# Optimization experiments

Measured on AMD Instinct MI355X. Metric: run time of the kernel, lower is better.

## Reference

```python
import jax, jax.numpy as jnp
import numpy as np

B, L, D = 4096, 16, 256  # batch, feat_len, feat_dim
N_ENC = 2                # common + synergy encoders


def _layer_norm(x, gamma, beta, eps=1e-5):
    m = jnp.mean(x, axis=-1, keepdims=True)
    v = jnp.mean(jnp.square(x - m), axis=-1, keepdims=True)
    return (x - m) * jax.lax.rsqrt(v + eps) * gamma + beta


def _estimator(gin, pin, Wg, bg, gng, gnb, Wp, bp, png, pnb, wga, bga, wpa, bpa):
    # MLP_Block = Linear + LayerNorm (Dropout is identity at inference)
    g = _layer_norm(jnp.einsum('bld,ed->ble', gin, Wg) + bg, gng, gnb)  # [B,L,D]
    p = _layer_norm(jnp.einsum('bld,ed->ble', pin, Wp) + bp, png, pnb)  # [B,L,D]
    # atten[b,l,i,j] = g[b,l,i]*p[b,l,j]
    # Linear(D,1) over j: sum_j wga_j*g_i*p_j + bga = g_i*(p.wga) + bga  (fused, no [B,L,D,D])
    geno_att = jax.nn.sigmoid(g * jnp.einsum('bld,d->bl', p, wga)[..., None] + bga)
    # permuted copy: atten.T over last two dims, Linear over i: p_j*(g.wpa) + bpa
    path_att = jax.nn.sigmoid(p * jnp.einsum('bld,d->bl', g, wpa)[..., None] + bpa)
    return p * path_att + g * geno_att


def setup_inputs() -> dict:
    key = jax.random.key(0)
    ks = jax.random.split(key, 8)
    s = 1.0 / np.sqrt(D)
    inp = {
        'gfeat': jax.random.normal(ks[0], (B, L, D), jnp.float32),
        'pfeat': jax.random.normal(ks[1], (B, L, D), jnp.float32),
        # stacked params for the 2 encoders (common, synergy)
        'Wg': jax.random.normal(ks[2], (N_ENC, D, D), jnp.float32) * s,
        'bg': jnp.zeros((N_ENC, D), jnp.float32),
        'gng': jnp.ones((N_ENC, D), jnp.float32),
        'gnb': jnp.zeros((N_ENC, D), jnp.float32),
        'Wp': jax.random.normal(ks[3], (N_ENC, D, D), jnp.float32) * s,
        'bp': jnp.zeros((N_ENC, D), jnp.float32),
        'png': jnp.ones((N_ENC, D), jnp.float32),
        'pnb': jnp.zeros((N_ENC, D), jnp.float32),
        'wga': jax.random.normal(ks[4], (N_ENC, D), jnp.float32) * s,
        'bga': jnp.zeros((N_ENC,), jnp.float32),
        'wpa': jax.random.normal(ks[5], (N_ENC, D), jnp.float32) * s,
        'bpa': jnp.zeros((N_ENC,), jnp.float32),
    }
    return inp


def reference(gfeat, pfeat, Wg, bg, gng, gnb, Wp, bp, png, pnb, wga, bga, wpa, bpa):
    # Knowledge_Decomposition calls both encoders as encoder(pfeat, gfeat) (swapped)
    est = jax.vmap(_estimator, in_axes=(None, None) + (0,) * 12)
    out = est(pfeat, gfeat, Wg, bg, gng, gnb, Wp, bp, png, pnb, wga, bga, wpa, bpa)  # [2,B,L,D]
    return (out[0], out[1])  # (common, synergy)
```

## Files before the change

### kernel.cpp

```cpp
#include <hip/hip_runtime.h>
#include <stdint.h>

typedef __bf16 bf16x8 __attribute__((ext_vector_type(8)));
typedef float  f32x4  __attribute__((ext_vector_type(4)));

#define BLD   16777216
#define DDIM  256

#define PARAM_OFF 0
#define STATS_OFF 8192
#define ROWC_OFF  16384
#define CONST_OFF 18432
#define SMEM_BYTES 18448

__device__ __forceinline__ float sigmoid_fast(float x){
  float e = __builtin_amdgcn_exp2f(-1.44269504f * x);
  return __builtin_amdgcn_rcpf(1.0f + e);
}

__device__ __forceinline__ bf16x8 cvt8(const float* p){
  float4 a = *(const float4*)p;
  float4 b = *(const float4*)(p + 4);
  bf16x8 r;
  r[0]=(__bf16)a.x; r[1]=(__bf16)a.y; r[2]=(__bf16)a.z; r[3]=(__bf16)a.w;
  r[4]=(__bf16)b.x; r[5]=(__bf16)b.y; r[6]=(__bf16)b.z; r[7]=(__bf16)b.w;
  return r;
}

__device__ __forceinline__ float ldp(const unsigned char* sm, int arr, int col){
  return ((const float*)(sm + PARAM_OFF))[arr*256 + col];
}

__global__ __launch_bounds__(256, 2)
void kd_kernel(const float* __restrict__ gfeat, const float* __restrict__ pfeat,
               const float* __restrict__ Wg,  const float* __restrict__ bg,
               const float* __restrict__ gng, const float* __restrict__ gnb,
               const float* __restrict__ Wp,  const float* __restrict__ bp,
               const float* __restrict__ pngm,const float* __restrict__ pnb,
               const float* __restrict__ wga, const float* __restrict__ bga,
               const float* __restrict__ wpa, const float* __restrict__ bpa,
               float* __restrict__ out)
{
  __shared__ __align__(16) unsigned char sm[SMEM_BYTES];
  const int tid  = threadIdx.x;
  const int n    = tid & 15;
  const int q    = (tid >> 4) & 3;
  const int w    = tid >> 6;
  const int tile = blockIdx.x >> 1;
  const int e    = blockIdx.x & 1;

  {
    float* pp = (float*)(sm + PARAM_OFF);
    pp[0*256 + tid] = bg  [e*256 + tid];
    pp[1*256 + tid] = gng [e*256 + tid];
    pp[2*256 + tid] = gnb [e*256 + tid];
    pp[3*256 + tid] = bp  [e*256 + tid];
    pp[4*256 + tid] = pngm[e*256 + tid];
    pp[5*256 + tid] = pnb [e*256 + tid];
    pp[6*256 + tid] = wga [e*256 + tid];
    pp[7*256 + tid] = wpa [e*256 + tid];
  }
  __syncthreads();

  if (tid < 64){
    float c0=0.f, c1=0.f, c2=0.f, c3=0.f;
    #pragma unroll
    for (int j = 0; j < 4; ++j){
      int c = tid*4 + j;
      float gng_ = ldp(sm,1,c), gnb_ = ldp(sm,2,c);
      float png_ = ldp(sm,4,c), pnb_ = ldp(sm,5,c);
      float wga_ = ldp(sm,6,c), wpa_ = ldp(sm,7,c);
      c0 += gng_*wpa_; c1 += gnb_*wpa_; c2 += png_*wga_; c3 += pnb_*wga_;
    }
    #pragma unroll
    for (int m = 1; m <= 32; m <<= 1){
      c0 += __shfl_xor(c0,m); c1 += __shfl_xor(c1,m);
      c2 += __shfl_xor(c2,m); c3 += __shfl_xor(c3,m);
    }
    if (tid == 0){
      float* cp = (float*)(sm + CONST_OFF);
      cp[0]=c0; cp[1]=c1; cp[2]=c2; cp[3]=c3;
    }
  }

  const float* aGbase = pfeat + (size_t)(tile*64 + n)*DDIM + q*8;
  const float* aPbase = gfeat + (size_t)(tile*64 + n)*DDIM + q*8;

  f32x4 accg[4][4], accp[4][4];
  #pragma unroll
  for (int t = 0; t < 4; ++t){
    int col = w*64 + n*4 + t;
    float bgv = ldp(sm,0,col);
    float bpv = ldp(sm,3,col);
    #pragma unroll
    for (int s = 0; s < 4; ++s){
      accg[s][t] = (f32x4){bgv,bgv,bgv,bgv};
      accp[s][t] = (f32x4){bpv,bpv,bpv,bpv};
    }
  }

  const float* wgE = Wg + (size_t)e*65536;
  const float* wpE = Wp + (size_t)e*65536;
  const float* wgR[4];
  const float* wpR[4];
  #pragma unroll
  for (int t = 0; t < 4; ++t){
    int row = w*64 + n*4 + t;
    wgR[t] = wgE + (size_t)row*DDIM + q*8;
    wpR[t] = wpE + (size_t)row*DDIM + q*8;
  }

  for (int kk = 0; kk < 8; ++kk){
    bf16x8 aG[4], aP[4], bG[4], bP[4];
    #pragma unroll
    for (int s = 0; s < 4; ++s){
      aG[s] = cvt8(aGbase + (size_t)s*16*DDIM + kk*32);
      aP[s] = cvt8(aPbase + (size_t)s*16*DDIM + kk*32);
    }
    #pragma unroll
    for (int t = 0; t < 4; ++t){
      bG[t] = cvt8(wgR[t] + kk*32);
      bP[t] = cvt8(wpR[t] + kk*32);
    }
    #pragma unroll
    for (int s = 0; s < 4; ++s){
      #pragma unroll
      for (int t = 0; t < 4; ++t){
        accg[s][t] = __builtin_amdgcn_mfma_f32_16x16x32_bf16(aG[s], bG[t], accg[s][t], 0,0,0);
        accp[s][t] = __builtin_amdgcn_mfma_f32_16x16x32_bf16(aP[s], bP[t], accp[s][t], 0,0,0);
      }
    }
  }

  float gamg[4], betg[4], gamp[4], betp[4], gwk[4], pwk[4];
  #pragma unroll
  for (int t = 0; t < 4; ++t){
    int col = w*64 + n*4 + t;
    float gng_ = ldp(sm,1,col), gnb_ = ldp(sm,2,col);
    float png_ = ldp(sm,4,col), pnb_ = ldp(sm,5,col);
    float wga_ = ldp(sm,6,col), wpa_ = ldp(sm,7,col);
    gamg[t]=gng_; betg[t]=gnb_; gamp[t]=png_; betp[t]=pnb_;
    gwk[t]=gng_*wpa_;
    pwk[t]=png_*wga_;
  }

  #pragma unroll
  for (int s = 0; s < 4; ++s){
    #pragma unroll
    for (int reg = 0; reg < 4; ++reg){
      float gs=0.f,gq=0.f,gw=0.f,ps=0.f,pq=0.f,pw=0.f;
      #pragma unroll
      for (int t = 0; t < 4; ++t){
        float xg = accg[s][t][reg], xp = accp[s][t][reg];
        gs += xg; gq = fmaf(xg,xg,gq); gw = fmaf(xg,gwk[t],gw);
        ps += xp; pq = fmaf(xp,xp,pq); pw = fmaf(xp,pwk[t],pw);
      }
      #pragma unroll
      for (int m = 1; m <= 8; m <<= 1){
        gs += __shfl_xor(gs,m); gq += __shfl_xor(gq,m); gw += __shfl_xor(gw,m);
        ps += __shfl_xor(ps,m); pq += __shfl_xor(pq,m); pw += __shfl_xor(pw,m);
      }
      if (n == 0){
        int r = s*16 + q*4 + reg;
        float* st = (float*)(sm + STATS_OFF) + (r*4 + w)*8;
        st[0]=gs; st[1]=gq; st[2]=gw; st[3]=ps; st[4]=pq; st[5]=pw;
      }
    }
  }
  __syncthreads();

  if (tid < 64){
    const float* cs = (const float*)(sm + CONST_OFF);
    float gs=0.f,gq=0.f,gw=0.f,ps=0.f,pq=0.f,pw=0.f;
    #pragma unroll
    for (int w2 = 0; w2 < 4; ++w2){
      const float* st = (const float*)(sm + STATS_OFF) + (tid*4 + w2)*8;
      gs+=st[0]; gq+=st[1]; gw+=st[2]; ps+=st[3]; pq+=st[4]; pw+=st[5];
    }
    float mg = gs*(1.f/256.f), vg = fmaxf(gq*(1.f/256.f) - mg*mg, 0.f);
    float rsg = rsqrtf(vg + 1e-5f);
    float mp = ps*(1.f/256.f), vp = fmaxf(pq*(1.f/256.f) - mp*mp, 0.f);
    float rsp = rsqrtf(vp + 1e-5f);
    float sp = rsg*(gw - mg*cs[0]) + cs[1];
    float sg = rsp*(pw - mp*cs[2]) + cs[3];
    float* rc = (float*)(sm + ROWC_OFF) + tid*8;
    rc[0]=mg; rc[1]=rsg; rc[2]=mp; rc[3]=rsp; rc[4]=sg; rc[5]=sp;
  }
  __syncthreads();

  const float bgaf = bga[e];
  const float bpaf = bpa[e];
  #pragma unroll
  for (int s = 0; s < 4; ++s){
    #pragma unroll
    for (int reg = 0; reg < 4; ++reg){
      int r = s*16 + q*4 + reg;
      const float* rc = (const float*)(sm + ROWC_OFF) + r*8;
      float mg=rc[0], rsg=rc[1], mp=rc[2], rsp=rc[3], sg=rc[4], sp=rc[5];
      float4 o;
      float ov[4];
      #pragma unroll
      for (int t = 0; t < 4; ++t){
        float g_ln = fmaf((accg[s][t][reg]-mg)*rsg, gamg[t], betg[t]);
        float p_ln = fmaf((accp[s][t][reg]-mp)*rsp, gamp[t], betp[t]);
        float ga = sigmoid_fast(fmaf(g_ln, sg, bgaf));
        float pa = sigmoid_fast(fmaf(p_ln, sp, bpaf));
        ov[t] = p_ln*pa + g_ln*ga;
      }
      o.x = ov[0]; o.y = ov[1]; o.z = ov[2]; o.w = ov[3];
      size_t off = (size_t)e*BLD + ((size_t)tile*64 + r)*DDIM + (w*64 + n*4);
      *(float4*)(out + off) = o;
    }
  }
}

extern "C" void kernel_launch(void* const* d_in, const int* in_sizes, int n_in,
                              void* d_out, int out_size, void* d_ws, size_t ws_size,
                              hipStream_t stream) {
  const float* gfeat = (const float*)d_in[0];
  const float* pfeat = (const float*)d_in[1];
  const float* Wg    = (const float*)d_in[2];
  const float* bg    = (const float*)d_in[3];
  const float* gng   = (const float*)d_in[4];
  const float* gnb   = (const float*)d_in[5];
  const float* Wp    = (const float*)d_in[6];
  const float* bp    = (const float*)d_in[7];
  const float* pngm  = (const float*)d_in[8];
  const float* pnb   = (const float*)d_in[9];
  const float* wga   = (const float*)d_in[10];
  const float* bga   = (const float*)d_in[11];
  const float* wpa   = (const float*)d_in[12];
  const float* bpa   = (const float*)d_in[13];

  dim3 grid(2048), block(256);
  hipLaunchKernelGGL(kd_kernel, grid, block, 0, stream,
                     gfeat, pfeat, Wg, bg, gng, gnb, Wp, bp, pngm, pnb,
                     wga, bga, wpa, bpa, (float*)d_out);
}
```

Before: 537.8 us.

## Stage activation tile in swizzled LDS as bf16 and halve rows per block

Each block now handles 32 rows instead of 64, doubling the grid. The block's activation tile is loaded once, converted to bf16 and stored in LDS with an XOR swizzle, and the MFMA A-fragments are read from LDS instead of being re-fetched from global memory per wave. The occupancy hint rises to 3 blocks per CU. The cost is a larger LDS footprint and an extra barrier. Weights are now re-read from global/L2 twice as often overall because tiles are smaller.

```diff
diff --git a/kernel.cpp b/kernel.cpp
--- a/kernel.cpp
+++ b/kernel.cpp
@@ -7,11 +7,13 @@
 #define BLD   16777216
 #define DDIM  256
 
-#define PARAM_OFF 0
-#define STATS_OFF 8192
-#define ROWC_OFF  16384
-#define CONST_OFF 18432
-#define SMEM_BYTES 18448
+#define AG_OFF    0
+#define AP_OFF    16384
+#define PARAM_OFF 32768
+#define STATS_OFF 40960
+#define ROWC_OFF  45056
+#define CONST_OFF 46080
+#define SMEM_BYTES 46096
 
 __device__ __forceinline__ float sigmoid_fast(float x){
   float e = __builtin_amdgcn_exp2f(-1.44269504f * x);
@@ -31,7 +33,7 @@
   return ((const float*)(sm + PARAM_OFF))[arr*256 + col];
 }
 
-__global__ __launch_bounds__(256, 2)
+__global__ __launch_bounds__(256, 3)
 void kd_kernel(const float* __restrict__ gfeat, const float* __restrict__ pfeat,
                const float* __restrict__ Wg,  const float* __restrict__ bg,
                const float* __restrict__ gng, const float* __restrict__ gnb,
@@ -49,6 +51,9 @@
   const int tile = blockIdx.x >> 1;
   const int e    = blockIdx.x & 1;
 
+  const int q16  = q*16;
+  const int xorv = (n & 7) << 4;
+
   {
     float* pp = (float*)(sm + PARAM_OFF);
     pp[0*256 + tid] = bg  [e*256 + tid];
@@ -60,6 +65,22 @@
     pp[6*256 + tid] = wga [e*256 + tid];
     pp[7*256 + tid] = wpa [e*256 + tid];
   }
+
+  {
+    const float* srcG = pfeat + (size_t)tile*32*DDIM;
+    const float* srcP = gfeat + (size_t)tile*32*DDIM;
+    #pragma unroll
+    for (int j = 0; j < 4; ++j){
+      int idx = j*2048 + tid*8;
+      int row = idx >> 8;
+      int col = idx & 255;
+      bf16x8 vg = cvt8(srcG + idx);
+      bf16x8 vp = cvt8(srcP + idx);
+      int off = row*512 + ((col*2) ^ ((row & 7) << 4));
+      *(bf16x8*)(sm + AG_OFF + off) = vg;
+      *(bf16x8*)(sm + AP_OFF + off) = vp;
+    }
+  }
   __syncthreads();
 
   if (tid < 64){
@@ -83,17 +104,14 @@
     }
   }
 
-  const float* aGbase = pfeat + (size_t)(tile*64 + n)*DDIM + q*8;
-  const float* aPbase = gfeat + (size_t)(tile*64 + n)*DDIM + q*8;
-
-  f32x4 accg[4][4], accp[4][4];
+  f32x4 accg[2][4], accp[2][4];
   #pragma unroll
   for (int t = 0; t < 4; ++t){
     int col = w*64 + n*4 + t;
     float bgv = ldp(sm,0,col);
     float bpv = ldp(sm,3,col);
     #pragma unroll
-    for (int s = 0; s < 4; ++s){
+    for (int s = 0; s < 2; ++s){
       accg[s][t] = (f32x4){bgv,bgv,bgv,bgv};
       accp[s][t] = (f32x4){bpv,bpv,bpv,bpv};
     }
@@ -101,29 +119,26 @@
 
   const float* wgE = Wg + (size_t)e*65536;
   const float* wpE = Wp + (size_t)e*65536;
-  const float* wgR[4];
-  const float* wpR[4];
-  #pragma unroll
-  for (int t = 0; t < 4; ++t){
-    int row = w*64 + n*4 + t;
-    wgR[t] = wgE + (size_t)row*DDIM + q*8;
-    wpR[t] = wpE + (size_t)row*DDIM + q*8;
-  }
+  int woff[4];
+  #pragma unroll
+  for (int t = 0; t < 4; ++t)
+    woff[t] = (w*64 + n*4 + t)*DDIM + q*8;
 
   for (int kk = 0; kk < 8; ++kk){
-    bf16x8 aG[4], aP[4], bG[4], bP[4];
-    #pragma unroll
-    for (int s = 0; s < 4; ++s){
-      aG[s] = cvt8(aGbase + (size_t)s*16*DDIM + kk*32);
-      aP[s] = cvt8(aPbase + (size_t)s*16*DDIM + kk*32);
+    bf16x8 aG[2], aP[2], bG[4], bP[4];
+    #pragma unroll
+    for (int s = 0; s < 2; ++s){
+      int off = (s*16 + n)*512 + ((kk*64 + q16) ^ xorv);
+      aG[s] = *(const bf16x8*)(sm + AG_OFF + off);
+      aP[s] = *(const bf16x8*)(sm + AP_OFF + off);
     }
     #pragma unroll
     for (int t = 0; t < 4; ++t){
-      bG[t] = cvt8(wgR[t] + kk*32);
-      bP[t] = cvt8(wpR[t] + kk*32);
-    }
-    #pragma unroll
-    for (int s = 0; s < 4; ++s){
+      bG[t] = cvt8(wgE + woff[t] + kk*32);
+      bP[t] = cvt8(wpE + woff[t] + kk*32);
+    }
+    #pragma unroll
+    for (int s = 0; s < 2; ++s){
       #pragma unroll
       for (int t = 0; t < 4; ++t){
         accg[s][t] = __builtin_amdgcn_mfma_f32_16x16x32_bf16(aG[s], bG[t], accg[s][t], 0,0,0);
@@ -145,7 +160,7 @@
   }
 
   #pragma unroll
-  for (int s = 0; s < 4; ++s){
+  for (int s = 0; s < 2; ++s){
     #pragma unroll
     for (int reg = 0; reg < 4; ++reg){
       float gs=0.f,gq=0.f,gw=0.f,ps=0.f,pq=0.f,pw=0.f;
@@ -169,7 +184,7 @@
   }
   __syncthreads();
 
-  if (tid < 64){
+  if (tid < 32){
     const float* cs = (const float*)(sm + CONST_OFF);
     float gs=0.f,gq=0.f,gw=0.f,ps=0.f,pq=0.f,pw=0.f;
     #pragma unroll
@@ -191,7 +206,7 @@
   const float bgaf = bga[e];
   const float bpaf = bpa[e];
   #pragma unroll
-  for (int s = 0; s < 4; ++s){
+  for (int s = 0; s < 2; ++s){
     #pragma unroll
     for (int reg = 0; reg < 4; ++reg){
       int r = s*16 + q*4 + reg;
@@ -208,7 +223,7 @@
         ov[t] = p_ln*pa + g_ln*ga;
       }
       o.x = ov[0]; o.y = ov[1]; o.z = ov[2]; o.w = ov[3];
-      size_t off = (size_t)e*BLD + ((size_t)tile*64 + r)*DDIM + (w*64 + n*4);
+      size_t off = (size_t)e*BLD + ((size_t)tile*32 + r)*DDIM + (w*64 + n*4);
       *(float4*)(out + off) = o;
     }
   }
@@ -232,7 +247,7 @@
   const float* wpa   = (const float*)d_in[12];
   const float* bpa   = (const float*)d_in[13];
 
-  dim3 grid(2048), block(256);
+  dim3 grid(4096), block(256);
   hipLaunchKernelGGL(kd_kernel, grid, block, 0, stream,
                      gfeat, pfeat, Wg, bg, gng, gnb, Wp, bp, pngm, pnb,
                      wga, bga, wpa, bpa, (float*)d_out);
```

New measurement: 453.6 us. 1.19x faster.

## Keep weights in registers and stage activation tiles in swizzled LDS across tiles

Applied to the files above, without the earlier changes.

The kernel now launches 256 blocks of 512 threads. Each block walks 4 row tiles for both encoders, and each wave keeps its 2-column slice of the bf16-converted weight matrices in registers, reloading them only when the encoder changes. Activation tiles are converted to bf16 once per tile, written into XOR-swizzled shared memory, and read from there by all waves, which removes the redundant per-wave global loads and fp32-to-bf16 conversions. In exchange, occupancy is much lower (one large block per CU, heavy register use), tile loads are not overlapped with compute, and each activation tile is still loaded twice, once per encoder.

```diff
diff --git a/kernel.cpp b/kernel.cpp
--- a/kernel.cpp
+++ b/kernel.cpp
@@ -6,12 +6,15 @@
 
 #define BLD   16777216
 #define DDIM  256
-
-#define PARAM_OFF 0
-#define STATS_OFF 8192
-#define ROWC_OFF  16384
-#define CONST_OFF 18432
-#define SMEM_BYTES 18448
+#define NT    4
+
+#define AG_OFF    0
+#define AP_OFF    32768
+#define PARAM_OFF 65536
+#define STATS_OFF 81920
+#define ROWC_OFF  100352
+#define CONST_OFF 102656
+#define SMEM_BYTES 102688
 
 __device__ __forceinline__ float sigmoid_fast(float x){
   float e = __builtin_amdgcn_exp2f(-1.44269504f * x);
@@ -27,11 +30,11 @@
   return r;
 }
 
-__device__ __forceinline__ float ldp(const unsigned char* sm, int arr, int col){
-  return ((const float*)(sm + PARAM_OFF))[arr*256 + col];
-}
-
-__global__ __launch_bounds__(256, 2)
+__device__ __forceinline__ float ldp(const unsigned char* sm, int e, int arr, int col){
+  return ((const float*)(sm + PARAM_OFF))[(e*8 + arr)*256 + col];
+}
+
+__global__ __launch_bounds__(512, 2)
 void kd_kernel(const float* __restrict__ gfeat, const float* __restrict__ pfeat,
                const float* __restrict__ Wg,  const float* __restrict__ bg,
                const float* __restrict__ gng, const float* __restrict__ gnb,
@@ -45,31 +48,50 @@
   const int tid  = threadIdx.x;
   const int n    = tid & 15;
   const int q    = (tid >> 4) & 3;
-  const int w    = tid >> 6;
-  const int tile = blockIdx.x >> 1;
-  const int e    = blockIdx.x & 1;
+  const int wv   = tid >> 6;
+  const int q16  = q*16;
+  const int xorv = (n & 7) << 4;
+  const int colb = wv*32 + n*2;
+  const int tb   = blockIdx.x * NT;
 
   {
-    float* pp = (float*)(sm + PARAM_OFF);
-    pp[0*256 + tid] = bg  [e*256 + tid];
-    pp[1*256 + tid] = gng [e*256 + tid];
-    pp[2*256 + tid] = gnb [e*256 + tid];
-    pp[3*256 + tid] = bp  [e*256 + tid];
-    pp[4*256 + tid] = pngm[e*256 + tid];
-    pp[5*256 + tid] = pnb [e*256 + tid];
-    pp[6*256 + tid] = wga [e*256 + tid];
-    pp[7*256 + tid] = wpa [e*256 + tid];
+    const int pe = tid >> 8, pc = tid & 255;
+    float* pp = (float*)(sm + PARAM_OFF) + pe*2048;
+    pp[0*256+pc] = bg  [pe*256+pc];
+    pp[1*256+pc] = gng [pe*256+pc];
+    pp[2*256+pc] = gnb [pe*256+pc];
+    pp[3*256+pc] = bp  [pe*256+pc];
+    pp[4*256+pc] = pngm[pe*256+pc];
+    pp[5*256+pc] = pnb [pe*256+pc];
+    pp[6*256+pc] = wga [pe*256+pc];
+    pp[7*256+pc] = wpa [pe*256+pc];
+  }
+
+  const int srow = tid >> 3;
+  const int scol = (tid & 7) * 8;
+
+  {
+    const float* pg = pfeat + ((size_t)tb*64 + srow)*DDIM;
+    const float* pv = gfeat + ((size_t)tb*64 + srow)*DDIM;
+    #pragma unroll
+    for (int c = 0; c < 4; ++c){
+      int col = scol + c*64;
+      int off = srow*512 + ((col*2) ^ ((srow & 7) << 4));
+      *(bf16x8*)(sm + AG_OFF + off) = cvt8(pg + col);
+      *(bf16x8*)(sm + AP_OFF + off) = cvt8(pv + col);
+    }
   }
   __syncthreads();
 
-  if (tid < 64){
+  if (tid < 128){
+    const int e2 = tid >> 6, l = tid & 63;
     float c0=0.f, c1=0.f, c2=0.f, c3=0.f;
     #pragma unroll
     for (int j = 0; j < 4; ++j){
-      int c = tid*4 + j;
-      float gng_ = ldp(sm,1,c), gnb_ = ldp(sm,2,c);
-      float png_ = ldp(sm,4,c), pnb_ = ldp(sm,5,c);
-      float wga_ = ldp(sm,6,c), wpa_ = ldp(sm,7,c);
+      int c = l*4 + j;
+      float gng_=ldp(sm,e2,1,c), gnb_=ldp(sm,e2,2,c);
+      float png_=ldp(sm,e2,4,c), pnb_=ldp(sm,e2,5,c);
+      float wga_=ldp(sm,e2,6,c), wpa_=ldp(sm,e2,7,c);
       c0 += gng_*wpa_; c1 += gnb_*wpa_; c2 += png_*wga_; c3 += pnb_*wga_;
     }
     #pragma unroll
@@ -77,139 +99,143 @@
       c0 += __shfl_xor(c0,m); c1 += __shfl_xor(c1,m);
       c2 += __shfl_xor(c2,m); c3 += __shfl_xor(c3,m);
     }
-    if (tid == 0){
-      float* cp = (float*)(sm + CONST_OFF);
+    if (l == 0){
+      float* cp = (float*)(sm + CONST_OFF) + e2*4;
       cp[0]=c0; cp[1]=c1; cp[2]=c2; cp[3]=c3;
     }
   }
 
-  const float* aGbase = pfeat + (size_t)(tile*64 + n)*DDIM + q*8;
-  const float* aPbase = gfeat + (size_t)(tile*64 + n)*DDIM + q*8;
-
-  f32x4 accg[4][4], accp[4][4];
-  #pragma unroll
-  for (int t = 0; t < 4; ++t){
-    int col = w*64 + n*4 + t;
-    float bgv = ldp(sm,0,col);
-    float bpv = ldp(sm,3,col);
+  bf16x8 wfG[8][2], wfP[8][2];
+  float biasG[2], gamG[2], betG[2], biasP[2], gamP[2], betP[2], gwk[2], pwk[2];
+  float attbG = 0.f, attbP = 0.f;
+
+  for (int rr = 0; rr < 2*NT; ++rr){
+    const int e    = rr >> 2;
+    const int tile = tb + (rr & 3);
+
+    if ((rr & 3) == 0){
+      const float* wgE = Wg + (size_t)e*65536;
+      const float* wpE = Wp + (size_t)e*65536;
+      #pragma unroll
+      for (int kk = 0; kk < 8; ++kk){
+        #pragma unroll
+        for (int t = 0; t < 2; ++t){
+          wfG[kk][t] = cvt8(wgE + (size_t)(colb + t)*DDIM + kk*32 + q*8);
+          wfP[kk][t] = cvt8(wpE + (size_t)(colb + t)*DDIM + kk*32 + q*8);
+        }
+      }
+      #pragma unroll
+      for (int t = 0; t < 2; ++t){
+        int col = colb + t;
+        biasG[t]=ldp(sm,e,0,col); gamG[t]=ldp(sm,e,1,col); betG[t]=ldp(sm,e,2,col);
+        biasP[t]=ldp(sm,e,3,col); gamP[t]=ldp(sm,e,4,col); betP[t]=ldp(sm,e,5,col);
+        float wgav=ldp(sm,e,6,col), wpav=ldp(sm,e,7,col);
+        gwk[t]=gamG[t]*wpav;
+        pwk[t]=gamP[t]*wgav;
+      }
+      attbG = bga[e]; attbP = bpa[e];
+    }
+
+    f32x4 accG[4][2], accP[4][2];
+    #pragma unroll
+    for (int s = 0; s < 4; ++s)
+      #pragma unroll
+      for (int t = 0; t < 2; ++t){
+        accG[s][t] = (f32x4){biasG[t],biasG[t],biasG[t],biasG[t]};
+        accP[s][t] = (f32x4){biasP[t],biasP[t],biasP[t],biasP[t]};
+      }
+    #pragma unroll
+    for (int kk = 0; kk < 8; ++kk){
+      const int co = (kk*64 + q16) ^ xorv;
+      #pragma unroll
+      for (int s = 0; s < 4; ++s){
+        bf16x8 aG = *(const bf16x8*)(sm + AG_OFF + (s*16 + n)*512 + co);
+        bf16x8 aP = *(const bf16x8*)(sm + AP_OFF + (s*16 + n)*512 + co);
+        #pragma unroll
+        for (int t = 0; t < 2; ++t){
+          accG[s][t] = __builtin_amdgcn_mfma_f32_16x16x32_bf16(aG, wfG[kk][t], accG[s][t], 0,0,0);
+          accP[s][t] = __builtin_amdgcn_mfma_f32_16x16x32_bf16(aP, wfP[kk][t], accP[s][t], 0,0,0);
+        }
+      }
+    }
+
     #pragma unroll
     for (int s = 0; s < 4; ++s){
-      accg[s][t] = (f32x4){bgv,bgv,bgv,bgv};
-      accp[s][t] = (f32x4){bpv,bpv,bpv,bpv};
-    }
-  }
-
-  const float* wgE = Wg + (size_t)e*65536;
-  const float* wpE = Wp + (size_t)e*65536;
-  const float* wgR[4];
-  const float* wpR[4];
-  #pragma unroll
-  for (int t = 0; t < 4; ++t){
-    int row = w*64 + n*4 + t;
-    wgR[t] = wgE + (size_t)row*DDIM + q*8;
-    wpR[t] = wpE + (size_t)row*DDIM + q*8;
-  }
-
-  for (int kk = 0; kk < 8; ++kk){
-    bf16x8 aG[4], aP[4], bG[4], bP[4];
+      #pragma unroll
+      for (int reg = 0; reg < 4; ++reg){
+        float gs=0.f,gq=0.f,gw=0.f,ps=0.f,pq=0.f,pw=0.f;
+        #pragma unroll
+        for (int t = 0; t < 2; ++t){
+          float xg = accG[s][t][reg], xp = accP[s][t][reg];
+          gs += xg; gq = fmaf(xg,xg,gq); gw = fmaf(xg,gwk[t],gw);
+          ps += xp; pq = fmaf(xp,xp,pq); pw = fmaf(xp,pwk[t],pw);
+        }
+        #pragma unroll
+        for (int m = 1; m <= 8; m <<= 1){
+          gs += __shfl_xor(gs,m); gq += __shfl_xor(gq,m); gw += __shfl_xor(gw,m);
+          ps += __shfl_xor(ps,m); pq += __shfl_xor(pq,m); pw += __shfl_xor(pw,m);
+        }
+        if (n == 0){
+          int r = s*16 + q*4 + reg;
+          float* st = (float*)(sm + STATS_OFF) + (wv*64 + r)*9;
+          st[0]=gs; st[1]=gq; st[2]=gw; st[3]=ps; st[4]=pq; st[5]=pw;
+        }
+      }
+    }
+    __syncthreads();
+
+    if (tid < 64){
+      const float* cs = (const float*)(sm + CONST_OFF) + e*4;
+      float gs=0.f,gq=0.f,gw=0.f,ps=0.f,pq=0.f,pw=0.f;
+      #pragma unroll
+      for (int w2 = 0; w2 < 8; ++w2){
+        const float* st = (const float*)(sm + STATS_OFF) + (w2*64 + tid)*9;
+        gs+=st[0]; gq+=st[1]; gw+=st[2]; ps+=st[3]; pq+=st[4]; pw+=st[5];
+      }
+      float mg = gs*(1.f/256.f), vg = fmaxf(gq*(1.f/256.f) - mg*mg, 0.f);
+      float rsg = rsqrtf(vg + 1e-5f);
+      float mp = ps*(1.f/256.f), vp = fmaxf(pq*(1.f/256.f) - mp*mp, 0.f);
+      float rsp = rsqrtf(vp + 1e-5f);
+      float spv = rsg*(gw - mg*cs[0]) + cs[1];
+      float sgv = rsp*(pw - mp*cs[2]) + cs[3];
+      float* rc = (float*)(sm + ROWC_OFF) + tid*9;
+      rc[0]=mg; rc[1]=rsg; rc[2]=mp; rc[3]=rsp; rc[4]=sgv; rc[5]=spv;
+    }
+    __syncthreads();
+
     #pragma unroll
     for (int s = 0; s < 4; ++s){
-      aG[s] = cvt8(aGbase + (size_t)s*16*DDIM + kk*32);
-      aP[s] = cvt8(aPbase + (size_t)s*16*DDIM + kk*32);
-    }
-    #pragma unroll
-    for (int t = 0; t < 4; ++t){
-      bG[t] = cvt8(wgR[t] + kk*32);
-      bP[t] = cvt8(wpR[t] + kk*32);
-    }
-    #pragma unroll
-    for (int s = 0; s < 4; ++s){
-      #pragma unroll
-      for (int t = 0; t < 4; ++t){
-        accg[s][t] = __builtin_amdgcn_mfma_f32_16x16x32_bf16(aG[s], bG[t], accg[s][t], 0,0,0);
-        accp[s][t] = __builtin_amdgcn_mfma_f32_16x16x32_bf16(aP[s], bP[t], accp[s][t], 0,0,0);
-      }
-    }
-  }
-
-  float gamg[4], betg[4], gamp[4], betp[4], gwk[4], pwk[4];
-  #pragma unroll
-  for (int t = 0; t < 4; ++t){
-    int col = w*64 + n*4 + t;
-    float gng_ = ldp(sm,1,col), gnb_ = ldp(sm,2,col);
-    float png_ = ldp(sm,4,col), pnb_ = ldp(sm,5,col);
-    float wga_ = ldp(sm,6,col), wpa_ = ldp(sm,7,col);
-    gamg[t]=gng_; betg[t]=gnb_; gamp[t]=png_; betp[t]=pnb_;
-    gwk[t]=gng_*wpa_;
-    pwk[t]=png_*wga_;
-  }
-
-  #pragma unroll
-  for (int s = 0; s < 4; ++s){
-    #pragma unroll
-    for (int reg = 0; reg < 4; ++reg){
-      float gs=0.f,gq=0.f,gw=0.f,ps=0.f,pq=0.f,pw=0.f;
-      #pragma unroll
-      for (int t = 0; t < 4; ++t){
-        float xg = accg[s][t][reg], xp = accp[s][t][reg];
-        gs += xg; gq = fmaf(xg,xg,gq); gw = fmaf(xg,gwk[t],gw);
-        ps += xp; pq = fmaf(xp,xp,pq); pw = fmaf(xp,pwk[t],pw);
-      }
-      #pragma unroll
-      for (int m = 1; m <= 8; m <<= 1){
-        gs += __shfl_xor(gs,m); gq += __shfl_xor(gq,m); gw += __shfl_xor(gw,m);
-        ps += __shfl_xor(ps,m); pq += __shfl_xor(pq,m); pw += __shfl_xor(pw,m);
-      }
-      if (n == 0){
+      #pragma unroll
+      for (int reg = 0; reg < 4; ++reg){
         int r = s*16 + q*4 + reg;
-        float* st = (float*)(sm + STATS_OFF) + (r*4 + w)*8;
-        st[0]=gs; st[1]=gq; st[2]=gw; st[3]=ps; st[4]=pq; st[5]=pw;
-      }
-    }
-  }
-  __syncthreads();
-
-  if (tid < 64){
-    const float* cs = (const float*)(sm + CONST_OFF);
-    float gs=0.f,gq=0.f,gw=0.f,ps=0.f,pq=0.f,pw=0.f;
-    #pragma unroll
-    for (int w2 = 0; w2 < 4; ++w2){
-      const float* st = (const float*)(sm + STATS_OFF) + (tid*4 + w2)*8;
-      gs+=st[0]; gq+=st[1]; gw+=st[2]; ps+=st[3]; pq+=st[4]; pw+=st[5];
-    }
-    float mg = gs*(1.f/256.f), vg = fmaxf(gq*(1.f/256.f) - mg*mg, 0.f);
-    float rsg = rsqrtf(vg + 1e-5f);
-    float mp = ps*(1.f/256.f), vp = fmaxf(pq*(1.f/256.f) - mp*mp, 0.f);
-    float rsp = rsqrtf(vp + 1e-5f);
-    float sp = rsg*(gw - mg*cs[0]) + cs[1];
-    float sg = rsp*(pw - mp*cs[2]) + cs[3];
-    float* rc = (float*)(sm + ROWC_OFF) + tid*8;
-    rc[0]=mg; rc[1]=rsg; rc[2]=mp; rc[3]=rsp; rc[4]=sg; rc[5]=sp;
-  }
-  __syncthreads();
-
-  const float bgaf = bga[e];
-  const float bpaf = bpa[e];
-  #pragma unroll
-  for (int s = 0; s < 4; ++s){
-    #pragma unroll
-    for (int reg = 0; reg < 4; ++reg){
-      int r = s*16 + q*4 + reg;
-      const float* rc = (const float*)(sm + ROWC_OFF) + r*8;
-      float mg=rc[0], rsg=rc[1], mp=rc[2], rsp=rc[3], sg=rc[4], sp=rc[5];
-      float4 o;
-      float ov[4];
-      #pragma unroll
-      for (int t = 0; t < 4; ++t){
-        float g_ln = fmaf((accg[s][t][reg]-mg)*rsg, gamg[t], betg[t]);
-        float p_ln = fmaf((accp[s][t][reg]-mp)*rsp, gamp[t], betp[t]);
-        float ga = sigmoid_fast(fmaf(g_ln, sg, bgaf));
-        float pa = sigmoid_fast(fmaf(p_ln, sp, bpaf));
-        ov[t] = p_ln*pa + g_ln*ga;
-      }
-      o.x = ov[0]; o.y = ov[1]; o.z = ov[2]; o.w = ov[3];
-      size_t off = (size_t)e*BLD + ((size_t)tile*64 + r)*DDIM + (w*64 + n*4);
-      *(float4*)(out + off) = o;
+        const float* rc = (const float*)(sm + ROWC_OFF) + r*9;
+        float mg=rc[0], rsg=rc[1], mp=rc[2], rsp=rc[3], sgv=rc[4], spv=rc[5];
+        float ov[2];
+        #pragma unroll
+        for (int t = 0; t < 2; ++t){
+          float g_ln = fmaf((accG[s][t][reg]-mg)*rsg, gamG[t], betG[t]);
+          float p_ln = fmaf((accP[s][t][reg]-mp)*rsp, gamP[t], betP[t]);
+          float ga = sigmoid_fast(fmaf(g_ln, sgv, attbG));
+          float pa = sigmoid_fast(fmaf(p_ln, spv, attbP));
+          ov[t] = p_ln*pa + g_ln*ga;
+        }
+        float2 o2; o2.x = ov[0]; o2.y = ov[1];
+        *(float2*)(out + (size_t)e*BLD + ((size_t)tile*64 + r)*DDIM + colb) = o2;
+      }
+    }
+
+    if (rr + 1 < 2*NT){
+      const int ti = tb + ((rr+1) & 3);
+      const float* pg = pfeat + ((size_t)ti*64 + srow)*DDIM;
+      const float* pv = gfeat + ((size_t)ti*64 + srow)*DDIM;
+      #pragma unroll
+      for (int c = 0; c < 4; ++c){
+        int col = scol + c*64;
+        int off = srow*512 + ((col*2) ^ ((srow & 7) << 4));
+        *(bf16x8*)(sm + AG_OFF + off) = cvt8(pg + col);
+        *(bf16x8*)(sm + AP_OFF + off) = cvt8(pv + col);
+      }
+      __syncthreads();
     }
   }
 }
@@ -232,7 +258,7 @@
   const float* wpa   = (const float*)d_in[12];
   const float* bpa   = (const float*)d_in[13];
 
-  dim3 grid(2048), block(256);
+  dim3 grid(256), block(512);
   hipLaunchKernelGGL(kd_kernel, grid, block, 0, stream,
                      gfeat, pfeat, Wg, bg, gng, gnb, Wp, bp, pngm, pnb,
                      wga, bga, wpa, bpa, (float*)d_out);
```

After: 451.2 us. 16.1% less time.
